# Kernel optimization log

Measured on AMD Instinct MI355X. Metric: run time of the kernel, lower is better.

Reference implementation:

```python
import jax, jax.numpy as jnp
import numpy as np
import math

H = 1024          # hidden_size
NH = 16           # num heads
HD = H // NH      # head_dim = 64
ORDER = 2         # torsion_order
RANK = 64         # torsion_rank


def setup_inputs() -> dict:
    key = jax.random.key(0)
    ks = jax.random.split(key, 16)
    B, S = 2, 2048
    std = 0.02
    inp = {
        "hidden_states": jax.random.normal(ks[0], (B, S, H), jnp.float32),
        # projection weights stored [in, out] (equivalent to torch Linear W^T)
        "Wq": jax.random.normal(ks[1], (H, H), jnp.float32) * std,
        "bq": jnp.zeros((H,), jnp.float32),
        "Wk": jax.random.normal(ks[2], (H, H), jnp.float32) * std,
        "bk": jnp.zeros((H,), jnp.float32),
        "Wv": jax.random.normal(ks[3], (H, H), jnp.float32) * std,
        "bv": jnp.zeros((H,), jnp.float32),
        "Wo": jax.random.normal(ks[4], (H, H), jnp.float32) * std,
        "bo": jnp.zeros((H,), jnp.float32),
        "q_torsion_a": jax.random.normal(ks[5], (ORDER, H, RANK), jnp.float32) * 0.01,
        "q_torsion_b": jax.random.normal(ks[6], (ORDER, RANK, H), jnp.float32) * 0.01,
        "k_torsion_a": jax.random.normal(ks[7], (ORDER, H, RANK), jnp.float32) * 0.01,
        "k_torsion_b": jax.random.normal(ks[8], (ORDER, RANK, H), jnp.float32) * 0.01,
        "torsion_coupling": jnp.asarray(0.1, jnp.float32),
    }
    return inp


def _apply_torsion(x, ta, tb, coupling):
    # x: [B,S,H]; ta: [ORDER,H,R]; tb: [ORDER,R,H]
    corr = jnp.zeros_like(x)
    for n in range(ORDER):
        low = jnp.einsum('bsh,hr->bsr', x, ta[n])
        lin = jnp.einsum('bsr,rh->bsh', low, tb[n])
        phase = (2.0 * math.pi * (n + 1)) * lin
        corr = corr + jnp.sin(phase) * lin / (n + 1)
    return x + jax.nn.sigmoid(coupling) * corr


def reference(hidden_states, Wq, bq, Wk, bk, Wv, bv, Wo, bo,
              q_torsion_a, q_torsion_b, k_torsion_a, k_torsion_b,
              torsion_coupling):
    B, S, _ = hidden_states.shape
    q = hidden_states @ Wq + bq
    k = hidden_states @ Wk + bk
    v = hidden_states @ Wv + bv
    q = _apply_torsion(q, q_torsion_a, q_torsion_b, torsion_coupling)
    k = _apply_torsion(k, k_torsion_a, k_torsion_b, torsion_coupling)
    # [B, NH, S, HD]
    q = q.reshape(B, S, NH, HD).transpose(0, 2, 1, 3)
    k = k.reshape(B, S, NH, HD).transpose(0, 2, 1, 3)
    v = v.reshape(B, S, NH, HD).transpose(0, 2, 1, 3)
    scale = HD ** -0.5
    attn = jnp.einsum('bhqd,bhkd->bhqk', q, k) * scale
    attn = jax.nn.softmax(attn, axis=-1)
    out = jnp.einsum('bhqk,bhkd->bhqd', attn, v)
    out = out.transpose(0, 2, 1, 3).reshape(B, S, H)
    return out @ Wo + bo
```

## Files before the change

kernel.cpp:

```cpp
#include <hip/hip_runtime.h>
#include <hip/hip_bf16.h>
#include <cstdint>
#include <cstddef>

typedef __bf16 bf16_t;
typedef __bf16 bf16x8 __attribute__((ext_vector_type(8)));
typedef float f32x4 __attribute__((ext_vector_type(4)));

static __device__ __forceinline__ void st_out(float* p, float v) { *p = v; }
static __device__ __forceinline__ void st_out(bf16_t* p, float v) { *p = (bf16_t)v; }

static __device__ __forceinline__ void async_cp16(const bf16_t* g, bf16_t* l) {
  __builtin_amdgcn_global_load_lds(
      (const __attribute__((address_space(1))) void*)g,
      (__attribute__((address_space(3))) void*)l, 16, 0, 0);
}

__global__ __launch_bounds__(256) void prep(const float* __restrict__ hs, bf16_t* __restrict__ hsb,
                                            const float* __restrict__ Wq, const float* __restrict__ Wk,
                                            const float* __restrict__ Wv, const float* __restrict__ Wo,
                                            bf16_t* __restrict__ BtExt, bf16_t* __restrict__ WoT,
                                            bf16_t* __restrict__ Wqb, bf16_t* __restrict__ Wkb,
                                            const float* __restrict__ qta, const float* __restrict__ kta,
                                            bf16_t* __restrict__ qtaT, bf16_t* __restrict__ ktaT,
                                            const float* __restrict__ qtb, const float* __restrict__ ktb,
                                            bf16_t* __restrict__ qtbT, bf16_t* __restrict__ ktbT,
                                            const float* __restrict__ bq, const float* __restrict__ bk,
                                            const float* __restrict__ bv, float* __restrict__ biasN) {
  __shared__ float tile[32][33];
  const int bid = blockIdx.x, t = threadIdx.x;
  const int tx = t & 31, ty = t >> 5;

  if (bid < 2048) {
    int i = (bid * 256 + t) * 8;
    float4 a = *(const float4*)(hs + i);
    float4 b = *(const float4*)(hs + i + 4);
    union { bf16_t h[8]; uint4 u; } p;
    p.h[0] = (bf16_t)a.x; p.h[1] = (bf16_t)a.y; p.h[2] = (bf16_t)a.z; p.h[3] = (bf16_t)a.w;
    p.h[4] = (bf16_t)b.x; p.h[5] = (bf16_t)b.y; p.h[6] = (bf16_t)b.z; p.h[7] = (bf16_t)b.w;
    *(uint4*)(hsb + i) = p.u;
  } else if (bid < 6144) {
    int r = bid - 2048, z = r >> 10, r10 = r & 1023;
    int bx = (r10 & 31) * 32, by = (r10 >> 5) * 32;
    const float* src = z == 0 ? Wq : z == 1 ? Wk : z == 2 ? Wv : Wo;
    bf16_t* dst = z == 3 ? WoT : BtExt + (size_t)z * 1048576;
    bf16_t* sd = z == 0 ? Wqb : z == 1 ? Wkb : nullptr;
#pragma unroll
    for (int i = 0; i < 4; ++i) {
      float v = src[(size_t)(by + ty + i * 8) * 1024 + bx + tx];
      tile[ty + i * 8][tx] = v;
      if (sd) sd[(size_t)(by + ty + i * 8) * 1024 + bx + tx] = (bf16_t)v;
    }
    __syncthreads();
#pragma unroll
    for (int i = 0; i < 4; ++i)
      dst[(size_t)(bx + ty + i * 8) * 1024 + by + tx] = (bf16_t)tile[tx][ty + i * 8];
  } else if (bid < 6400) {
    int r = bid - 6144, z = r >> 6, r6 = r & 63;
    int bx = (r6 & 1) * 32, by = (r6 >> 1) * 32;
    const float* src = ((z >> 1) ? kta : qta) + (size_t)(z & 1) * 65536;
    bf16_t* dst = ((z >> 1) ? ktaT : qtaT) + (size_t)(z & 1) * 65536;
#pragma unroll
    for (int i = 0; i < 4; ++i)
      tile[ty + i * 8][tx] = src[(size_t)(by + ty + i * 8) * 64 + bx + tx];
    __syncthreads();
#pragma unroll
    for (int i = 0; i < 4; ++i)
      dst[(size_t)(bx + ty + i * 8) * 1024 + by + tx] = (bf16_t)tile[tx][ty + i * 8];
  } else if (bid < 6656) {
    int r = bid - 6400, z = r >> 6, r6 = r & 63;
    int bx = (r6 & 31) * 32, by = (r6 >> 5) * 32;
    const float* src = ((z >> 1) ? ktb : qtb) + (size_t)(z & 1) * 65536;
    bf16_t* dst = ((z >> 1) ? ktbT : qtbT) + (size_t)(z & 1) * 65536;
#pragma unroll
    for (int i = 0; i < 4; ++i)
      tile[ty + i * 8][tx] = src[(size_t)(by + ty + i * 8) * 1024 + bx + tx];
    __syncthreads();
#pragma unroll
    for (int i = 0; i < 4; ++i)
      dst[(size_t)(bx + ty + i * 8) * 64 + by + tx] = (bf16_t)tile[tx][ty + i * 8];
  } else if (bid < 6668) {
    int i = (bid - 6656) * 256 + t;
    biasN[i] = (i < 1024) ? bq[i] : (i < 2048 ? bk[i - 1024] : bv[i - 2048]);
  } else {
    int j = t;
    const float* b = (j < 128) ? bq : bk;
    const float* ta = ((j < 128) ? qta : kta) + (size_t)((j >> 6) & 1) * 65536;
    int rr = j & 63;
    float s = 0.f;
    for (int h = 0; h < 1024; ++h) s += b[h] * ta[(size_t)h * 64 + rr];
    biasN[3072 + j] = s;
  }
}

template <typename OutT>
static __device__ __forceinline__ void gemm_core_async(const bf16_t* __restrict__ A, int lda,
                                                       const bf16_t* __restrict__ Bt, int ldb,
                                                       OutT* __restrict__ C, int ldc,
                                                       const float* __restrict__ bias, int K,
                                                       int bx, int by) {
  __shared__ bf16_t As[128][32];
  __shared__ bf16_t Bs[128][32];
  const int m0 = by * 128, n0 = bx * 128;
  const int t = threadIdx.x, w = t >> 6, lane = t & 63;
  const int wm = (w >> 1) * 64, wn = (w & 1) * 64;
  const int quad = lane >> 4, l16 = lane & 15;
  const int sra = lane >> 2, sca = (lane & 3) * 8;
  const bf16_t* Ag0 = A + (size_t)(m0 + w * 16 + sra) * lda + sca;
  const bf16_t* Ag1 = A + (size_t)(m0 + 64 + w * 16 + sra) * lda + sca;
  const bf16_t* Bg0 = Bt + (size_t)(n0 + w * 16 + sra) * ldb + sca;
  const bf16_t* Bg1 = Bt + (size_t)(n0 + 64 + w * 16 + sra) * ldb + sca;
  bf16_t* la0 = &As[0][0] + w * 512;
  bf16_t* la1 = &As[0][0] + 2048 + w * 512;
  bf16_t* lb0 = &Bs[0][0] + w * 512;
  bf16_t* lb1 = &Bs[0][0] + 2048 + w * 512;

  f32x4 acc[4][4] = {};
  for (int k0 = 0; k0 < K; k0 += 32) {
    __syncthreads();
    async_cp16(Ag0 + k0, la0);
    async_cp16(Ag1 + k0, la1);
    async_cp16(Bg0 + k0, lb0);
    async_cp16(Bg1 + k0, lb1);
    __syncthreads();
    bf16x8 af[4], bfr[4];
#pragma unroll
    for (int i = 0; i < 4; ++i)
      af[i] = *(const bf16x8*)&As[wm + i * 16 + l16][quad * 8];
#pragma unroll
    for (int j = 0; j < 4; ++j)
      bfr[j] = *(const bf16x8*)&Bs[wn + j * 16 + l16][quad * 8];
#pragma unroll
    for (int i = 0; i < 4; ++i)
#pragma unroll
      for (int j = 0; j < 4; ++j)
        acc[i][j] = __builtin_amdgcn_mfma_f32_16x16x32_bf16(af[i], bfr[j], acc[i][j], 0, 0, 0);
  }
#pragma unroll
  for (int i = 0; i < 4; ++i) {
    int row = m0 + wm + i * 16 + quad * 4;
#pragma unroll
    for (int j = 0; j < 4; ++j) {
      int col = n0 + wn + j * 16 + l16;
      float bv = bias ? bias[col] : 0.f;
#pragma unroll
      for (int r = 0; r < 4; ++r)
        st_out(&C[(size_t)(row + r) * ldc + col], acc[i][j][r] + bv);
    }
  }
}

template <typename OutT>
static __device__ __forceinline__ void gemm_core_async64(const bf16_t* __restrict__ A, int lda,
                                                         const bf16_t* __restrict__ Bt, int ldb,
                                                         OutT* __restrict__ C, int ldc,
                                                         const float* __restrict__ bias, int K,
                                                         int bx, int by) {
  __shared__ bf16_t As[64][32];
  __shared__ bf16_t Bs[128][32];
  const int m0 = by * 64, n0 = bx * 128;
  const int t = threadIdx.x, w = t >> 6, lane = t & 63;
  const int wm = (w >> 1) * 32, wn = (w & 1) * 64;
  const int quad = lane >> 4, l16 = lane & 15;
  const int sra = lane >> 2, sca = (lane & 3) * 8;
  const bf16_t* Ag0 = A + (size_t)(m0 + w * 16 + sra) * lda + sca;
  const bf16_t* Bg0 = Bt + (size_t)(n0 + w * 16 + sra) * ldb + sca;
  const bf16_t* Bg1 = Bt + (size_t)(n0 + 64 + w * 16 + sra) * ldb + sca;
  bf16_t* la0 = &As[0][0] + w * 512;
  bf16_t* lb0 = &Bs[0][0] + w * 512;
  bf16_t* lb1 = &Bs[0][0] + 2048 + w * 512;

  f32x4 acc[2][4] = {};
  for (int k0 = 0; k0 < K; k0 += 32) {
    __syncthreads();
    async_cp16(Ag0 + k0, la0);
    async_cp16(Bg0 + k0, lb0);
    async_cp16(Bg1 + k0, lb1);
    __syncthreads();
    bf16x8 af[2], bfr[4];
#pragma unroll
    for (int i = 0; i < 2; ++i)
      af[i] = *(const bf16x8*)&As[wm + i * 16 + l16][quad * 8];
#pragma unroll
    for (int j = 0; j < 4; ++j)
      bfr[j] = *(const bf16x8*)&Bs[wn + j * 16 + l16][quad * 8];
#pragma unroll
    for (int i = 0; i < 2; ++i)
#pragma unroll
      for (int j = 0; j < 4; ++j)
        acc[i][j] = __builtin_amdgcn_mfma_f32_16x16x32_bf16(af[i], bfr[j], acc[i][j], 0, 0, 0);
  }
#pragma unroll
  for (int i = 0; i < 2; ++i) {
    int row = m0 + wm + i * 16 + quad * 4;
#pragma unroll
    for (int j = 0; j < 4; ++j) {
      int col = n0 + wn + j * 16 + l16;
      float bv = bias ? bias[col] : 0.f;
#pragma unroll
      for (int r = 0; r < 4; ++r)
        st_out(&C[(size_t)(row + r) * ldc + col], acc[i][j][r] + bv);
    }
  }
}

__global__ __launch_bounds__(256) void gemm_qkv(const bf16_t* __restrict__ A,
                                                const bf16_t* __restrict__ Bt,
                                                bf16_t* __restrict__ C,
                                                const float* __restrict__ biasN) {
  int id = blockIdx.y * 26 + blockIdx.x;
  int nid = (id & 7) * 104 + (id >> 3);
  gemm_core_async<bf16_t>(A, 1024, Bt, 1024, C, 3328, biasN, 1024, nid % 26, nid / 26);
}

__global__ __launch_bounds__(256) void gemm_out(const bf16_t* __restrict__ A,
                                                const bf16_t* __restrict__ Bt,
                                                float* __restrict__ C,
                                                const float* __restrict__ bo) {
  int id = blockIdx.y * 8 + blockIdx.x;
  int nid = (id & 7) * 64 + (id >> 3);
  gemm_core_async64<float>(A, 1024, Bt, 1024, C, 1024, bo, 1024, nid & 7, nid >> 3);
}

__global__ __launch_bounds__(256) void gemm_wta(const bf16_t* __restrict__ qtaT,
                                                const bf16_t* __restrict__ ktaT,
                                                const bf16_t* __restrict__ Wqb,
                                                const bf16_t* __restrict__ Wkb,
                                                bf16_t* __restrict__ BtExt) {
  int z = blockIdx.z;
  gemm_core_async64<bf16_t>(z ? ktaT : qtaT, 1024, z ? Wkb : Wqb, 1024,
                            BtExt + (size_t)(3072 + z * 128) * 1024, 1024,
                            nullptr, 1024, blockIdx.x, blockIdx.y);
}

__global__ __launch_bounds__(256) void lin_torsion_fused(const bf16_t* __restrict__ qtbT,
                                                         const bf16_t* __restrict__ ktbT,
                                                         bf16_t* __restrict__ qkv,
                                                         const float* __restrict__ coupling) {
  __shared__ bf16_t As[128][136];
  __shared__ bf16_t Bs0[128][72];
  __shared__ bf16_t Bs1[128][72];
  const int z = blockIdx.z;
  const bf16_t* Low = qkv + 3072 + z * 128;
  const bf16_t* Tb = z ? ktbT : qtbT;
  bf16_t* X = qkv + z * 1024;

  const int m0 = blockIdx.y * 128, n0 = blockIdx.x * 128;
  const int t = threadIdx.x, w = t >> 6, lane = t & 63;
  const int wm = (w >> 1) * 64, wn = (w & 1) * 64;
  const int quad = lane >> 4, l16 = lane & 15;

  {
    const int sr = t >> 1, sc = (t & 1) * 64;
    const bf16_t* Ag = Low + (size_t)(m0 + sr) * 3328 + sc;
#pragma unroll
    for (int i = 0; i < 8; ++i)
      *(float4*)&As[sr][sc + 8 * i] = *(const float4*)(Ag + 8 * i);
    const int br = t >> 1, bc = (t & 1) * 32;
    const bf16_t* Bg0 = Tb + (size_t)(n0 + br) * 64 + bc;
    const bf16_t* Bg1 = Bg0 + 65536;
#pragma unroll
    for (int i = 0; i < 4; ++i) {
      *(float4*)&Bs0[br][bc + 8 * i] = *(const float4*)(Bg0 + 8 * i);
      *(float4*)&Bs1[br][bc + 8 * i] = *(const float4*)(Bg1 + 8 * i);
    }
  }
  __syncthreads();

  f32x4 acc0[4][4] = {}, acc1[4][4] = {};
#pragma unroll
  for (int ks = 0; ks < 2; ++ks) {
    bf16x8 a0[4], a1[4];
#pragma unroll
    for (int i = 0; i < 4; ++i) {
      a0[i] = *(const bf16x8*)&As[wm + i * 16 + l16][ks * 32 + quad * 8];
      a1[i] = *(const bf16x8*)&As[wm + i * 16 + l16][64 + ks * 32 + quad * 8];
    }
#pragma unroll
    for (int j = 0; j < 4; ++j) {
      bf16x8 b0 = *(const bf16x8*)&Bs0[wn + j * 16 + l16][ks * 32 + quad * 8];
      bf16x8 b1 = *(const bf16x8*)&Bs1[wn + j * 16 + l16][ks * 32 + quad * 8];
#pragma unroll
      for (int i = 0; i < 4; ++i) {
        acc0[i][j] = __builtin_amdgcn_mfma_f32_16x16x32_bf16(a0[i], b0, acc0[i][j], 0, 0, 0);
        acc1[i][j] = __builtin_amdgcn_mfma_f32_16x16x32_bf16(a1[i], b1, acc1[i][j], 0, 0, 0);
      }
    }
  }

  const float PI2 = 6.283185307179586f;
  const float sig = 1.f / (1.f + __expf(-coupling[0]));
  const float scale = z ? 1.f : 0.1803368801111204f;
#pragma unroll
  for (int i = 0; i < 4; ++i) {
#pragma unroll
    for (int j = 0; j < 4; ++j) {
#pragma unroll
      for (int r = 0; r < 4; ++r) {
        int row = m0 + wm + i * 16 + quad * 4 + r;
        int col = n0 + wn + j * 16 + l16;
        size_t idx = (size_t)row * 3328 + col;
        float l1 = acc0[i][j][r], l2 = acc1[i][j][r];
        float corr = __sinf(PI2 * l1) * l1 + __sinf(2.f * PI2 * l2) * l2 * 0.5f;
        X[idx] = (bf16_t)(((float)X[idx] + sig * corr) * scale);
      }
    }
  }
}

__global__ __launch_bounds__(256, 2) void flash_attn(const bf16_t* __restrict__ qkv,
                                                     bf16_t* __restrict__ aout) {
  constexpr int LD = 3328, SEQ = 2048;
  const int qb = blockIdx.x, bh = blockIdx.y;
  const int b = bh >> 4, h = bh & 15;
  const size_t base = (size_t)b * SEQ * LD + h * 64;
  const bf16_t* Qg = qkv + base;
  const bf16_t* Kg = qkv + base + 1024;
  const bf16_t* Vg = qkv + base + 2048;

  __shared__ __align__(16) unsigned char smem[67584];
  bf16_t(*VT0)[136] = (bf16_t(*)[136])smem;
  bf16_t(*VT1)[136] = (bf16_t(*)[136])(smem + 17408);
  bf16_t* Kl0 = (bf16_t*)(smem + 34816);
  bf16_t* Kl1 = (bf16_t*)(smem + 51200);
  float* LDSo = (float*)smem;
  float* Lred = (float*)(smem + 24576);
  float* invL = (float*)(smem + 28672);

  const int t = threadIdx.x, w = t >> 6, lane = t & 63;
  const int kw = w >> 1, qw = w & 1;
  const int quad = lane >> 4, l16 = lane & 15;
  const int q0 = qb * 128;

  bf16x8 qf[4][2];
  {
    const bf16_t* Qrow = Qg + (size_t)(q0 + qw * 64 + l16) * LD + quad * 8;
#pragma unroll
    for (int nf = 0; nf < 4; ++nf)
#pragma unroll
      for (int ks = 0; ks < 2; ++ks)
        qf[nf][ks] = *(const bf16x8*)(Qrow + (size_t)(nf * 16) * LD + ks * 32);
  }

  f32x4 o[4][4] = {};
  float l_part[4] = {0.f, 0.f, 0.f, 0.f};

  const int vg = t >> 3, vcb = (t & 7) * 8;
  const int colb = (((vg >> 3) << 5) | ((vg & 3) << 3) | (((vg >> 2) & 1) << 2)) ^ ((t & 7) << 3);
  const bf16_t* Vbase = Vg + (size_t)(vg * 4) * LD + vcb;

  const bf16_t* Kstg = Kg + (size_t)(w * 8 + (lane >> 3)) * LD + ((lane & 7) ^ (lane >> 3)) * 8;

  float4 vr[4];

  {
    bf16_t* dst = Kl0 + w * 512;
#pragma unroll
    for (int c = 0; c < 4; ++c)
      async_cp16(Kstg + (size_t)(c * 32) * LD, dst + c * 2048);
  }
#pragma unroll
  for (int kk = 0; kk < 4; ++kk)
    vr[kk] = *(const float4*)(Vbase + (size_t)kk * LD);
#pragma unroll
  for (int cc = 0; cc < 8; ++cc) {
    union { bf16_t h[4]; uint2 u; } pk;
#pragma unroll
    for (int kk = 0; kk < 4; ++kk) pk.h[kk] = ((const bf16_t*)&vr[kk])[cc];
    *(uint2*)&VT0[vcb + cc][colb] = pk.u;
  }
#pragma unroll
  for (int kk = 0; kk < 4; ++kk)
    vr[kk] = *(const float4*)(Vbase + (size_t)(128 + kk) * LD);
  __syncthreads();

  for (int k0 = 0; k0 < SEQ; k0 += 128) {
    const int cur = (k0 >> 7) & 1;
    bf16_t(*VTc)[136] = cur ? VT1 : VT0;
    bf16_t(*VTn)[136] = cur ? VT0 : VT1;
    const bf16_t* Kc = cur ? Kl1 : Kl0;

    if (k0 + 128 < SEQ) {
      bf16_t* dst = (cur ? Kl0 : Kl1) + w * 512;
#pragma unroll
      for (int c = 0; c < 4; ++c)
        async_cp16(Kstg + (size_t)(k0 + 128 + c * 32) * LD, dst + c * 2048);
    }

    bf16x8 kf[4][2];
#pragma unroll
    for (int jk = 0; jk < 4; ++jk) {
      int row = kw * 64 + jk * 16 + l16;
#pragma unroll
      for (int ks = 0; ks < 2; ++ks) {
        int ch = (ks * 4 + quad) ^ (l16 & 7);
        kf[jk][ks] = *(const bf16x8*)&Kc[row * 64 + ch * 8];
      }
    }

    f32x4 st[4][4] = {};
    __builtin_amdgcn_s_setprio(1);
#pragma unroll
    for (int ks = 0; ks < 2; ++ks)
#pragma unroll
      for (int jk = 0; jk < 4; ++jk)
#pragma unroll
        for (int nf = 0; nf < 4; ++nf)
          st[jk][nf] = __builtin_amdgcn_mfma_f32_16x16x32_bf16(kf[jk][ks], qf[nf][ks], st[jk][nf], 0, 0, 0);
    __builtin_amdgcn_s_setprio(0);

    bf16x8 Pp[2][4];
#pragma unroll
    for (int g = 0; g < 2; ++g)
#pragma unroll
      for (int nf = 0; nf < 4; ++nf) {
        union { bf16_t hh[8]; bf16x8 v; } ph;
#pragma unroll
        for (int b2 = 0; b2 < 2; ++b2)
#pragma unroll
          for (int r = 0; r < 4; ++r) {
            float p = exp2f(st[g * 2 + b2][nf][r]);
            l_part[nf] += p;
            ph.hh[b2 * 4 + r] = (bf16_t)p;
          }
        Pp[g][nf] = ph.v;
      }

    if (k0 + 128 < SEQ) {
#pragma unroll
      for (int cc = 0; cc < 8; ++cc) {
        union { bf16_t h[4]; uint2 u; } pk;
#pragma unroll
        for (int kk = 0; kk < 4; ++kk) pk.h[kk] = ((const bf16_t*)&vr[kk])[cc];
        *(uint2*)&VTn[vcb + cc][colb] = pk.u;
      }
      if (k0 + 256 < SEQ) {
#pragma unroll
        for (int kk = 0; kk < 4; ++kk)
          vr[kk] = *(const float4*)(Vbase + (size_t)(k0 + 256 + kk) * LD);
      }
    }

#pragma unroll
    for (int g = 0; g < 2; ++g) {
      bf16x8 vf[4];
#pragma unroll
      for (int jd = 0; jd < 4; ++jd) {
        int row = jd * 16 + l16;
        int col = (kw * 64 + g * 32 + quad * 8) ^ ((((row >> 3) & 7)) << 3);
        vf[jd] = *(const bf16x8*)&VTc[row][col];
      }
      __builtin_amdgcn_s_setprio(1);
#pragma unroll
      for (int jd = 0; jd < 4; ++jd)
#pragma unroll
        for (int nf = 0; nf < 4; ++nf)
          o[jd][nf] = __builtin_amdgcn_mfma_f32_16x16x32_bf16(vf[jd], Pp[g][nf], o[jd][nf], 0, 0, 0);
      __builtin_amdgcn_s_setprio(0);
    }

    __builtin_amdgcn_sched_barrier(0);
    if (k0 + 256 < SEQ)
      asm volatile("s_waitcnt vmcnt(4) lgkmcnt(0)" ::: "memory");
    else
      asm volatile("s_waitcnt vmcnt(0) lgkmcnt(0)" ::: "memory");
    __builtin_amdgcn_s_barrier();
    __builtin_amdgcn_sched_barrier(0);
  }

#pragma unroll
  for (int nf = 0; nf < 4; ++nf)
    Lred[((kw * 2 + qw) * 4 + quad) * 64 + nf * 16 + l16] = l_part[nf];
  __syncthreads();
  if (t < 128) {
    int qw2 = t >> 6, ql = t & 63;
    float s = 0.f;
#pragma unroll
    for (int kw2 = 0; kw2 < 2; ++kw2)
#pragma unroll
      for (int qd = 0; qd < 4; ++qd)
        s += Lred[((kw2 * 2 + qw2) * 4 + qd) * 64 + ql];
    invL[t] = 1.f / s;
  }
  __syncthreads();

  const int rq = t >> 1, rc0 = (t & 1) * 8;
#pragma unroll
  for (int jd = 0; jd < 4; ++jd) {
#pragma unroll
    for (int nf = 0; nf < 4; ++nf)
      *(f32x4*)&LDSo[(size_t)(kw * 128 + qw * 64 + nf * 16 + l16) * 24 + quad * 4] = o[jd][nf];
    __syncthreads();
    f32x4 a0 = *(const f32x4*)&LDSo[(size_t)rq * 24 + rc0];
    f32x4 a1 = *(const f32x4*)&LDSo[(size_t)(128 + rq) * 24 + rc0];
    f32x4 b0 = *(const f32x4*)&LDSo[(size_t)rq * 24 + rc0 + 4];
    f32x4 b1 = *(const f32x4*)&LDSo[(size_t)(128 + rq) * 24 + rc0 + 4];
    float iv = invL[rq];
    union { bf16_t h[8]; uint4 u; } pk;
#pragma unroll
    for (int r = 0; r < 4; ++r) {
      pk.h[r] = (bf16_t)((a0[r] + a1[r]) * iv);
      pk.h[4 + r] = (bf16_t)((b0[r] + b1[r]) * iv);
    }
    *(uint4*)&aout[(size_t)(b * SEQ + q0 + rq) * 1024 + h * 64 + jd * 16 + rc0] = pk.u;
    if (jd < 3) __syncthreads();
  }
}

extern "C" void kernel_launch(void* const* d_in, const int* in_sizes, int n_in,
                              void* d_out, int out_size, void* d_ws, size_t ws_size,
                              hipStream_t stream) {
  const float* hs   = (const float*)d_in[0];
  const float* Wq   = (const float*)d_in[1];
  const float* bq   = (const float*)d_in[2];
  const float* Wk   = (const float*)d_in[3];
  const float* bk   = (const float*)d_in[4];
  const float* Wv   = (const float*)d_in[5];
  const float* bv   = (const float*)d_in[6];
  const float* Wo   = (const float*)d_in[7];
  const float* bo   = (const float*)d_in[8];
  const float* qta  = (const float*)d_in[9];
  const float* qtb  = (const float*)d_in[10];
  const float* kta  = (const float*)d_in[11];
  const float* ktb  = (const float*)d_in[12];
  const float* coup = (const float*)d_in[13];
  float* out = (float*)d_out;

  uint8_t* ws = (uint8_t*)d_ws;
  bf16_t* hsb   = (bf16_t*)(ws);
  bf16_t* aout  = (bf16_t*)(ws);
  bf16_t* BtExt = (bf16_t*)(ws + 8388608);
  bf16_t* WoT   = (bf16_t*)(ws + 16777216);
  float*  biasN = (float*)(ws + 18874368);
  bf16_t* qkv   = (bf16_t*)(ws + 18890752);
  bf16_t* Wqb   = (bf16_t*)(ws + 46153728);
  bf16_t* Wkb   = (bf16_t*)(ws + 48250880);
  bf16_t* qtaT  = (bf16_t*)(ws + 50348032);
  bf16_t* ktaT  = (bf16_t*)(ws + 50610176);
  bf16_t* qtbT  = (bf16_t*)(ws + 50872320);
  bf16_t* ktbT  = (bf16_t*)(ws + 51134464);

  dim3 b256(256);

  prep<<<6669, b256, 0, stream>>>(hs, hsb, Wq, Wk, Wv, Wo, BtExt, WoT, Wqb, Wkb,
                                  qta, kta, qtaT, ktaT, qtb, ktb, qtbT, ktbT,
                                  bq, bk, bv, biasN);
  gemm_wta<<<dim3(8, 2, 2), b256, 0, stream>>>(qtaT, ktaT, Wqb, Wkb, BtExt);
  gemm_qkv<<<dim3(26, 32), b256, 0, stream>>>(hsb, BtExt, qkv, biasN);
  lin_torsion_fused<<<dim3(8, 32, 2), b256, 0, stream>>>(qtbT, ktbT, qkv, coup);
  flash_attn<<<dim3(16, 32), b256, 0, stream>>>(qkv, aout);
  gemm_out<<<dim3(8, 64), b256, 0, stream>>>(aout, WoT, out, bo);
}
```

Before: 282.7 us.

## Use BK=64 XOR-swizzled GEMM core and parallelize torsion bias reduction

Replaces the BK=32 GEMM core with a BK=64 version whose LDS tiles use an XOR swizzle on 16-byte chunks, halving the number of barrier pairs per K and reducing LDS bank conflicts. The output projection moves from a 64-row core to the 128x128 core, which halves its grid. The single-block serial torsion bias reduction (256 threads each looping over 1024) becomes 16 blocks, each using 16-lane partial sums combined by shuffles. In exchange the GEMM uses more LDS per block, which may lower occupancy, and the smaller output grid may underfill the GPU.

Result: faster. 261.7 us, median of 2 (-7.4%).

```diff
diff --git a/kernel.cpp b/kernel.cpp
--- a/kernel.cpp
+++ b/kernel.cpp
@@ -83,58 +83,68 @@
     int i = (bid - 6656) * 256 + t;
     biasN[i] = (i < 1024) ? bq[i] : (i < 2048 ? bk[i - 1024] : bv[i - 2048]);
   } else {
-    int j = t;
+    int B = bid - 6668;
+    int j = B * 16 + (t >> 4);
+    int hoff = t & 15;
     const float* b = (j < 128) ? bq : bk;
     const float* ta = ((j < 128) ? qta : kta) + (size_t)((j >> 6) & 1) * 65536;
     int rr = j & 63;
     float s = 0.f;
-    for (int h = 0; h < 1024; ++h) s += b[h] * ta[(size_t)h * 64 + rr];
-    biasN[3072 + j] = s;
+#pragma unroll 4
+    for (int i = 0; i < 64; ++i) {
+      int h = hoff + i * 16;
+      s += b[h] * ta[(size_t)h * 64 + rr];
+    }
+#pragma unroll
+    for (int m = 8; m >= 1; m >>= 1) s += __shfl_xor(s, m, 64);
+    if (hoff == 0) biasN[3072 + j] = s;
   }
 }
 
 template <typename OutT>
-static __device__ __forceinline__ void gemm_core_async(const bf16_t* __restrict__ A, int lda,
-                                                       const bf16_t* __restrict__ Bt, int ldb,
-                                                       OutT* __restrict__ C, int ldc,
-                                                       const float* __restrict__ bias, int K,
-                                                       int bx, int by) {
-  __shared__ bf16_t As[128][32];
-  __shared__ bf16_t Bs[128][32];
+static __device__ __forceinline__ void gemm_core_bk64(const bf16_t* __restrict__ A, int lda,
+                                                      const bf16_t* __restrict__ Bt, int ldb,
+                                                      OutT* __restrict__ C, int ldc,
+                                                      const float* __restrict__ bias, int K,
+                                                      int bx, int by) {
+  __shared__ bf16_t As[128][64];
+  __shared__ bf16_t Bs[128][64];
   const int m0 = by * 128, n0 = bx * 128;
   const int t = threadIdx.x, w = t >> 6, lane = t & 63;
   const int wm = (w >> 1) * 64, wn = (w & 1) * 64;
   const int quad = lane >> 4, l16 = lane & 15;
-  const int sra = lane >> 2, sca = (lane & 3) * 8;
-  const bf16_t* Ag0 = A + (size_t)(m0 + w * 16 + sra) * lda + sca;
-  const bf16_t* Ag1 = A + (size_t)(m0 + 64 + w * 16 + sra) * lda + sca;
-  const bf16_t* Bg0 = Bt + (size_t)(n0 + w * 16 + sra) * ldb + sca;
-  const bf16_t* Bg1 = Bt + (size_t)(n0 + 64 + w * 16 + sra) * ldb + sca;
-  bf16_t* la0 = &As[0][0] + w * 512;
-  bf16_t* la1 = &As[0][0] + 2048 + w * 512;
-  bf16_t* lb0 = &Bs[0][0] + w * 512;
-  bf16_t* lb1 = &Bs[0][0] + 2048 + w * 512;
+  const int sra = lane >> 3;
+  const int sch = lane & 7;
+  const bf16_t* Ag = A + (size_t)(m0 + w * 32 + sra) * lda + (sch ^ sra) * 8;
+  const bf16_t* Bg = Bt + (size_t)(n0 + w * 32 + sra) * ldb + (sch ^ sra) * 8;
+  bf16_t* la = &As[0][0] + w * 2048;
+  bf16_t* lb = &Bs[0][0] + w * 2048;
 
   f32x4 acc[4][4] = {};
-  for (int k0 = 0; k0 < K; k0 += 32) {
-    __syncthreads();
-    async_cp16(Ag0 + k0, la0);
-    async_cp16(Ag1 + k0, la1);
-    async_cp16(Bg0 + k0, lb0);
-    async_cp16(Bg1 + k0, lb1);
-    __syncthreads();
-    bf16x8 af[4], bfr[4];
-#pragma unroll
-    for (int i = 0; i < 4; ++i)
-      af[i] = *(const bf16x8*)&As[wm + i * 16 + l16][quad * 8];
-#pragma unroll
-    for (int j = 0; j < 4; ++j)
-      bfr[j] = *(const bf16x8*)&Bs[wn + j * 16 + l16][quad * 8];
-#pragma unroll
-    for (int i = 0; i < 4; ++i)
+  for (int k0 = 0; k0 < K; k0 += 64) {
+    __syncthreads();
+#pragma unroll
+    for (int c = 0; c < 4; ++c)
+      async_cp16(Ag + k0 + (size_t)(c * 8) * lda, la + c * 512);
+#pragma unroll
+    for (int c = 0; c < 4; ++c)
+      async_cp16(Bg + k0 + (size_t)(c * 8) * ldb, lb + c * 512);
+    __syncthreads();
+#pragma unroll
+    for (int ks = 0; ks < 2; ++ks) {
+      bf16x8 af[4], bfr[4];
+#pragma unroll
+      for (int i = 0; i < 4; ++i)
+        af[i] = *(const bf16x8*)&As[wm + i * 16 + l16][((ks * 4 + quad) ^ (l16 & 7)) * 8];
 #pragma unroll
       for (int j = 0; j < 4; ++j)
-        acc[i][j] = __builtin_amdgcn_mfma_f32_16x16x32_bf16(af[i], bfr[j], acc[i][j], 0, 0, 0);
+        bfr[j] = *(const bf16x8*)&Bs[wn + j * 16 + l16][((ks * 4 + quad) ^ (l16 & 7)) * 8];
+#pragma unroll
+      for (int i = 0; i < 4; ++i)
+#pragma unroll
+        for (int j = 0; j < 4; ++j)
+          acc[i][j] = __builtin_amdgcn_mfma_f32_16x16x32_bf16(af[i], bfr[j], acc[i][j], 0, 0, 0);
+    }
   }
 #pragma unroll
   for (int i = 0; i < 4; ++i) {
@@ -210,7 +220,7 @@
                                                 const float* __restrict__ biasN) {
   int id = blockIdx.y * 26 + blockIdx.x;
   int nid = (id & 7) * 104 + (id >> 3);
-  gemm_core_async<bf16_t>(A, 1024, Bt, 1024, C, 3328, biasN, 1024, nid % 26, nid / 26);
+  gemm_core_bk64<bf16_t>(A, 1024, Bt, 1024, C, 3328, biasN, 1024, nid % 26, nid / 26);
 }
 
 __global__ __launch_bounds__(256) void gemm_out(const bf16_t* __restrict__ A,
@@ -218,8 +228,8 @@
                                                 float* __restrict__ C,
                                                 const float* __restrict__ bo) {
   int id = blockIdx.y * 8 + blockIdx.x;
-  int nid = (id & 7) * 64 + (id >> 3);
-  gemm_core_async64<float>(A, 1024, Bt, 1024, C, 1024, bo, 1024, nid & 7, nid >> 3);
+  int nid = (id & 7) * 32 + (id >> 3);
+  gemm_core_bk64<float>(A, 1024, Bt, 1024, C, 1024, bo, 1024, nid & 7, nid >> 3);
 }
 
 __global__ __launch_bounds__(256) void gemm_wta(const bf16_t* __restrict__ qtaT,
@@ -542,12 +552,12 @@
 
   dim3 b256(256);
 
-  prep<<<6669, b256, 0, stream>>>(hs, hsb, Wq, Wk, Wv, Wo, BtExt, WoT, Wqb, Wkb,
+  prep<<<6684, b256, 0, stream>>>(hs, hsb, Wq, Wk, Wv, Wo, BtExt, WoT, Wqb, Wkb,
                                   qta, kta, qtaT, ktaT, qtb, ktb, qtbT, ktbT,
                                   bq, bk, bv, biasN);
   gemm_wta<<<dim3(8, 2, 2), b256, 0, stream>>>(qtaT, ktaT, Wqb, Wkb, BtExt);
   gemm_qkv<<<dim3(26, 32), b256, 0, stream>>>(hsb, BtExt, qkv, biasN);
   lin_torsion_fused<<<dim3(8, 32, 2), b256, 0, stream>>>(qtbT, ktbT, qkv, coup);
   flash_attn<<<dim3(16, 32), b256, 0, stream>>>(qkv, aout);
-  gemm_out<<<dim3(8, 64), b256, 0, stream>>>(aout, WoT, out, bo);
-}
+  gemm_out<<<dim3(8, 32), b256, 0, stream>>>(aout, WoT, out, bo);
+}
```
